# Kernel optimization log

Measured on AMD Instinct MI355X. Metric: run time of the kernel, lower is better.

## Reference

```python
import jax, jax.numpy as jnp
import numpy as np

H, W = 512, 512  # image_size from init_kwargs


def _render_single(xyz, color, opacity):
    """Faithful JAX version of GaussianRenderer._fallback_render (the path the
    module executes when the CUDA rasterizer is unavailable), vectorized.
    Point-splat each Gaussian to one pixel, depth-sort descending (back-to-front),
    alpha-composite: a_k = o_k * prod_{j<k}(1 - o_j); depth = z of front-most hit.
    xyz: (N,3)  color: (N,3)  opacity: (N,1)
    """
    N = xyz.shape[0]
    focal = (H + W) / 2.0
    z = xyz[:, 2]
    xf = xyz[:, 0] / (z + 1e-6) * focal + W / 2.0
    yf = xyz[:, 1] / (z + 1e-6) * focal + H / 2.0
    # torch .long() truncates toward zero
    xi = jnp.trunc(jnp.clip(xf, -1e9, 1e9)).astype(jnp.int32)
    yi = jnp.trunc(jnp.clip(yf, -1e9, 1e9)).astype(jnp.int32)
    valid = (xi >= 0) & (xi < W) & (yi >= 0) & (yi < H)
    pix = jnp.where(valid, yi * W + xi, H * W)  # dummy slot H*W for out-of-bounds
    # stable sort: primary pixel ascending, secondary z descending (back-to-front)
    order = jnp.lexsort((-z, pix))
    pix_s, z_s = pix[order], z[order]
    o_s = opacity[order, 0]
    c_s = color[order]
    valid_s = pix_s < H * W
    # per-pixel exclusive transmittance: alpha recurrence 1-A_k = (1-A_{k-1})(1-o_k)
    logt = jnp.log(jnp.clip(1.0 - o_s, 1e-12, None))
    cs = jnp.cumsum(logt)
    excl = cs - logt  # exclusive cumsum (global)
    start = jnp.concatenate([jnp.ones((1,), bool), pix_s[1:] != pix_s[:-1]])
    start_idx = jax.lax.cummax(jnp.where(start, jnp.arange(N), -1))
    T_prev = jnp.exp(excl - excl[start_idx])  # exclusive within pixel segment
    a = jnp.where(valid_s, o_s * T_prev, 0.0)
    img = jnp.zeros((H * W + 1, 3), xyz.dtype).at[pix_s].add(a[:, None] * c_s)
    # depth: last element written per pixel (front-most, smallest z in segment)
    end = jnp.concatenate([pix_s[1:] != pix_s[:-1], jnp.ones((1,), bool)])
    dpix = jnp.where(end & valid_s, pix_s, H * W)
    depth = jnp.zeros((H * W + 1,), xyz.dtype).at[dpix].set(z_s)
    render = img[: H * W].reshape(H, W, 3).transpose(2, 0, 1)  # (3,H,W)
    return render, depth[: H * W].reshape(1, H, W)


def setup_inputs() -> dict:
    key = jax.random.key(0)
    ks = jax.random.split(key, 5)
    B, N = 8, 262144
    return {
        "xyz": jax.random.normal(ks[0], (B, N, 3), jnp.float32),
        "scale": jax.random.normal(ks[1], (B, N, 3), jnp.float32),
        "rotation": jax.random.normal(ks[2], (B, N, 1), jnp.float32),
        "opacity": jax.random.uniform(ks[3], (B, N, 1), jnp.float32),
        "color": jax.random.uniform(ks[4], (B, N, 3), jnp.float32),
    }


def reference(xyz, scale, rotation, opacity, color):
    # scale/rotation are accepted (part of the gaussians dict) but unused by the
    # fallback renderer, matching the torch source.
    render, depth = jax.vmap(_render_single)(xyz, color, opacity)
    return render, depth
```

## Files before the change

### kernel.cpp

```cpp
#include <hip/hip_runtime.h>
#include <stdint.h>

#define W_ 512
#define H_ 512
#define HW_ (512 * 512)
#define RMAX 4
#define OVF_CAP 65536

__device__ __forceinline__ int project_pix(float x, float y, float z) {
    float zz = z + 1e-6f;
    float xf = x / zz * 512.0f + 256.0f;
    float yf = y / zz * 512.0f + 256.0f;
    xf = fminf(fmaxf(xf, -1e9f), 1e9f);
    yf = fminf(fmaxf(yf, -1e9f), 1e9f);
    int xi = (int)xf;
    int yi = (int)yf;
    if (xi >= 0 && xi < W_ && yi >= 0 && yi < H_) return yi * W_ + xi;
    return -1;
}

__device__ __forceinline__ unsigned int q8(float v) {
    v = fminf(fmaxf(v, 0.f), 1.f);
    return (unsigned int)__float2uint_rn(v * 255.0f);
}
__device__ __forceinline__ float d8(unsigned int u) {
    return (float)(u & 255u) * (1.0f / 255.0f);
}

__global__ void __launch_bounds__(256) k_init(uint4* __restrict__ p, int n4) {
    int i = blockIdx.x * blockDim.x + threadIdx.x;
    if (i < n4) p[i] = make_uint4(0u, 0u, 0u, 0u);
}

__global__ void __launch_bounds__(256) k_build(const float4* __restrict__ xyz4,
                                               const float4* __restrict__ op4,
                                               const float4* __restrict__ col4,
                                               unsigned int* __restrict__ cnt,
                                               unsigned long long* __restrict__ slots,
                                               unsigned int* __restrict__ ovf_hdr,
                                               unsigned int* __restrict__ ovf_pix,
                                               unsigned long long* __restrict__ ovf_rec,
                                               int N, int total4) {
    int t = blockIdx.x * blockDim.x + threadIdx.x;
    if (t >= total4) return;
    float4 v0 = xyz4[3 * (size_t)t + 0];
    float4 v1 = xyz4[3 * (size_t)t + 1];
    float4 v2 = xyz4[3 * (size_t)t + 2];
    float4 o4 = op4[t];
    float4 c0 = col4[3 * (size_t)t + 0];
    float4 c1 = col4[3 * (size_t)t + 1];
    float4 c2 = col4[3 * (size_t)t + 2];
    float xs[4] = {v0.x, v0.w, v1.z, v2.y};
    float ys[4] = {v0.y, v1.x, v1.w, v2.z};
    float zs[4] = {v0.z, v1.y, v2.x, v2.w};
    float os[4] = {o4.x, o4.y, o4.z, o4.w};
    float cr[4] = {c0.x, c0.w, c1.z, c2.y};
    float cg[4] = {c0.y, c1.x, c1.w, c2.z};
    float cb[4] = {c0.z, c1.y, c2.x, c2.w};
    int g0 = 4 * t;
    size_t pbase = (size_t)(g0 / N) * HW_;
#pragma unroll
    for (int j = 0; j < 4; ++j) {
        int pix = project_pix(xs[j], ys[j], zs[j]);
        if (pix >= 0) {
            size_t p = pbase + pix;
            unsigned int sh = 16u * (unsigned int)(p & 1);
            unsigned int old = atomicAdd(&cnt[p >> 1], 1u << sh);
            unsigned int s = (old >> sh) & 0xffffu;
            unsigned int pay = q8(os[j]) | (q8(cr[j]) << 8) | (q8(cg[j]) << 16) |
                               (q8(cb[j]) << 24);
            unsigned long long rec =
                ((unsigned long long)__float_as_uint(zs[j]) << 32) | (unsigned long long)pay;
            if (s < RMAX) {
                slots[p * RMAX + s] = rec;
            } else {
                unsigned int i = atomicAdd(ovf_hdr, 1u);
                if (i < OVF_CAP) { ovf_pix[i] = (unsigned int)p; ovf_rec[i] = rec; }
            }
        }
    }
}

__global__ void __launch_bounds__(256) k_composite(const unsigned int* __restrict__ cnt,
                                                   const unsigned long long* __restrict__ slots,
                                                   const unsigned int* __restrict__ ovf_hdr,
                                                   const unsigned int* __restrict__ ovf_pix,
                                                   const unsigned long long* __restrict__ ovf_rec,
                                                   float* __restrict__ out, int B) {
    int q = blockIdx.x * blockDim.x + threadIdx.x;
    int nb8 = B * (HW_ / 8);
    if (q >= nb8) return;
    int p0 = 8 * q;
    int b = p0 / HW_;
    int pl0 = p0 - b * HW_;

    uint4 cw = ((const uint4*)cnt)[q];
    unsigned int ws[4] = {cw.x, cw.y, cw.z, cw.w};

    float rr[8], gg[8], bb[8], dd[8];

#pragma unroll
    for (int j = 0; j < 8; ++j) {
        unsigned int k = (ws[j >> 1] >> (16 * (j & 1))) & 0xffffu;
        float r = 0.f, g2 = 0.f, bl = 0.f, depth = 0.f;
        if (k > 0) {
            size_t p = (size_t)p0 + j;
            const uint4* sp = (const uint4*)&slots[p * RMAX];
            uint4 s01 = sp[0];
            if (k <= RMAX) {
                uint4 s23 = (k > 2) ? sp[1]
                                    : make_uint4(~0u, 0xff800000u, ~0u, 0xff800000u);
                float z_[4];
                unsigned int y_[4];
                z_[0] = __uint_as_float(s01.y); y_[0] = s01.x;
                z_[1] = (k > 1) ? __uint_as_float(s01.w) : -__builtin_inff();
                y_[1] = s01.z;
                z_[2] = __uint_as_float(s23.y); y_[2] = s23.x;
                z_[3] = (k > 3) ? __uint_as_float(s23.w) : -__builtin_inff();
                y_[3] = s23.z;
#define CE(I, J)                                                                \
                {                                                               \
                    bool sw = (z_[J] > z_[I]) || (z_[J] == z_[I] && y_[J] < y_[I]); \
                    if (sw) {                                                   \
                        float tz = z_[I]; z_[I] = z_[J]; z_[J] = tz;            \
                        unsigned int ty = y_[I]; y_[I] = y_[J]; y_[J] = ty;     \
                    }                                                           \
                }
                CE(0,1) CE(2,3) CE(0,2) CE(1,3) CE(1,2)
#undef CE
                float T = 1.f;
#pragma unroll
                for (int s = 0; s < RMAX; ++s) {
                    if (s < (int)k) {
                        unsigned int pay = y_[s];
                        float o = d8(pay);
                        float a = o * T;
                        r  += a * d8(pay >> 8);
                        g2 += a * d8(pay >> 16);
                        bl += a * d8(pay >> 24);
                        T *= (1.0f - o);
                        depth = z_[s];
                    }
                }
            } else {
                uint4 s23 = sp[1];
                unsigned int nov = ovf_hdr[0];
                if (nov > OVF_CAP) nov = OVF_CAP;
                unsigned int ptag = (unsigned int)p;
                float zz0 = __uint_as_float(s01.y), zz1 = __uint_as_float(s01.w);
                float zz2 = __uint_as_float(s23.y), zz3 = __uint_as_float(s23.w);
                float prev_z = __builtin_inff();
                unsigned int prev_y = 0u;
                float T = 1.f;
                for (int s = 0; s < (int)k; ++s) {
                    float best_z = -__builtin_inff();
                    unsigned int best_y = ~0u;
#define CAND(Z, Y)                                                                   \
                    {                                                                \
                        float z = (Z); unsigned int y = (Y);                         \
                        bool after  = (z < prev_z) || (z == prev_z && y > prev_y);   \
                        bool better = (z > best_z) || (z == best_z && y < best_y);   \
                        if (after && better) { best_z = z; best_y = y; }             \
                    }
                    CAND(zz0, s01.x) CAND(zz1, s01.z) CAND(zz2, s23.x) CAND(zz3, s23.z)
                    for (unsigned int t2 = 0; t2 < nov; ++t2) {
                        if (ovf_pix[t2] == ptag) {
                            unsigned long long rec = ovf_rec[t2];
                            CAND(__uint_as_float((unsigned int)(rec >> 32)),
                                 (unsigned int)rec)
                        }
                    }
#undef CAND
                    unsigned int pay = best_y;
                    float o = d8(pay);
                    float a = o * T;
                    r  += a * d8(pay >> 8);
                    g2 += a * d8(pay >> 16);
                    bl += a * d8(pay >> 24);
                    T *= (1.0f - o);
                    depth = best_z;
                    prev_z = best_z;
                    prev_y = best_y;
                }
            }
        }
        rr[j] = r; gg[j] = g2; bb[j] = bl; dd[j] = depth;
    }

    size_t HWs = (size_t)HW_;
    float* oR = out + ((size_t)b * 3 + 0) * HWs + pl0;
    float* oG = out + ((size_t)b * 3 + 1) * HWs + pl0;
    float* oB = out + ((size_t)b * 3 + 2) * HWs + pl0;
    float* oD = out + (size_t)B * 3 * HWs + (size_t)b * HWs + pl0;
    *(float4*)(oR)     = make_float4(rr[0], rr[1], rr[2], rr[3]);
    *(float4*)(oR + 4) = make_float4(rr[4], rr[5], rr[6], rr[7]);
    *(float4*)(oG)     = make_float4(gg[0], gg[1], gg[2], gg[3]);
    *(float4*)(oG + 4) = make_float4(gg[4], gg[5], gg[6], gg[7]);
    *(float4*)(oB)     = make_float4(bb[0], bb[1], bb[2], bb[3]);
    *(float4*)(oB + 4) = make_float4(bb[4], bb[5], bb[6], bb[7]);
    *(float4*)(oD)     = make_float4(dd[0], dd[1], dd[2], dd[3]);
    *(float4*)(oD + 4) = make_float4(dd[4], dd[5], dd[6], dd[7]);
}

extern "C" void kernel_launch(void* const* d_in, const int* in_sizes, int n_in,
                              void* d_out, int out_size, void* d_ws, size_t ws_size,
                              hipStream_t stream) {
    const float* xyz     = (const float*)d_in[0];
    const float* opacity = (const float*)d_in[3];
    const float* color   = (const float*)d_in[4];
    float* out = (float*)d_out;

    int B = out_size / (4 * HW_);
    int N = in_sizes[0] / (3 * B);
    int total = B * N;
    int nb = B * HW_;

    unsigned int* cnt      = (unsigned int*)d_ws;
    unsigned int* ovf_hdr  = cnt + nb / 2;
    unsigned int* ovf_pix  = ovf_hdr + 64;
    unsigned long long* ovf_rec = (unsigned long long*)(ovf_pix + OVF_CAP);
    unsigned long long* slots   = ovf_rec + OVF_CAP;

    int blk = 256;
    int zwords = nb / 2 + 64;
    int z4 = zwords / 4;
    k_init<<<(z4 + blk - 1) / blk, blk, 0, stream>>>((uint4*)cnt, z4);

    int total4 = total / 4;
    k_build<<<(total4 + blk - 1) / blk, blk, 0, stream>>>((const float4*)xyz,
                                                          (const float4*)opacity,
                                                          (const float4*)color,
                                                          cnt, slots, ovf_hdr, ovf_pix, ovf_rec,
                                                          N, total4);

    int nb8 = nb / 8;
    k_composite<<<(nb8 + blk - 1) / blk, blk, 0, stream>>>(cnt, slots, ovf_hdr, ovf_pix,
                                                           ovf_rec, out, B);
}
```

Measured before the change: 43.06 us.

## Split compositing into zero-fill scan plus compacted work-queue pass

After: 90.15 us. 109% more time.

```diff
diff --git a/kernel.cpp b/kernel.cpp
--- a/kernel.cpp
+++ b/kernel.cpp
@@ -37,7 +37,7 @@
                                                const float4* __restrict__ col4,
                                                unsigned int* __restrict__ cnt,
                                                unsigned long long* __restrict__ slots,
-                                               unsigned int* __restrict__ ovf_hdr,
+                                               unsigned int* __restrict__ hdr,
                                                unsigned int* __restrict__ ovf_pix,
                                                unsigned long long* __restrict__ ovf_rec,
                                                int N, int total4) {
@@ -74,18 +74,16 @@
             if (s < RMAX) {
                 slots[p * RMAX + s] = rec;
             } else {
-                unsigned int i = atomicAdd(ovf_hdr, 1u);
+                unsigned int i = atomicAdd(&hdr[0], 1u);
                 if (i < OVF_CAP) { ovf_pix[i] = (unsigned int)p; ovf_rec[i] = rec; }
             }
         }
     }
 }
 
-__global__ void __launch_bounds__(256) k_composite(const unsigned int* __restrict__ cnt,
-                                                   const unsigned long long* __restrict__ slots,
-                                                   const unsigned int* __restrict__ ovf_hdr,
-                                                   const unsigned int* __restrict__ ovf_pix,
-                                                   const unsigned long long* __restrict__ ovf_rec,
+__global__ void __launch_bounds__(256) k_zero_scan(const unsigned int* __restrict__ cnt,
+                                                   unsigned int* __restrict__ qn,
+                                                   unsigned int* __restrict__ queue,
                                                    float* __restrict__ out, int B) {
     int q = blockIdx.x * blockDim.x + threadIdx.x;
     int nb8 = B * (HW_ / 8);
@@ -97,109 +95,147 @@
     uint4 cw = ((const uint4*)cnt)[q];
     unsigned int ws[4] = {cw.x, cw.y, cw.z, cw.w};
 
-    float rr[8], gg[8], bb[8], dd[8];
-
-#pragma unroll
-    for (int j = 0; j < 8; ++j) {
-        unsigned int k = (ws[j >> 1] >> (16 * (j & 1))) & 0xffffu;
-        float r = 0.f, g2 = 0.f, bl = 0.f, depth = 0.f;
-        if (k > 0) {
-            size_t p = (size_t)p0 + j;
-            const uint4* sp = (const uint4*)&slots[p * RMAX];
-            uint4 s01 = sp[0];
-            if (k <= RMAX) {
-                uint4 s23 = (k > 2) ? sp[1]
-                                    : make_uint4(~0u, 0xff800000u, ~0u, 0xff800000u);
-                float z_[4];
-                unsigned int y_[4];
-                z_[0] = __uint_as_float(s01.y); y_[0] = s01.x;
-                z_[1] = (k > 1) ? __uint_as_float(s01.w) : -__builtin_inff();
-                y_[1] = s01.z;
-                z_[2] = __uint_as_float(s23.y); y_[2] = s23.x;
-                z_[3] = (k > 3) ? __uint_as_float(s23.w) : -__builtin_inff();
-                y_[3] = s23.z;
-#define CE(I, J)                                                                \
-                {                                                               \
-                    bool sw = (z_[J] > z_[I]) || (z_[J] == z_[I] && y_[J] < y_[I]); \
-                    if (sw) {                                                   \
-                        float tz = z_[I]; z_[I] = z_[J]; z_[J] = tz;            \
-                        unsigned int ty = y_[I]; y_[I] = y_[J]; y_[J] = ty;     \
-                    }                                                           \
-                }
-                CE(0,1) CE(2,3) CE(0,2) CE(1,3) CE(1,2)
-#undef CE
-                float T = 1.f;
-#pragma unroll
-                for (int s = 0; s < RMAX; ++s) {
-                    if (s < (int)k) {
-                        unsigned int pay = y_[s];
-                        float o = d8(pay);
-                        float a = o * T;
-                        r  += a * d8(pay >> 8);
-                        g2 += a * d8(pay >> 16);
-                        bl += a * d8(pay >> 24);
-                        T *= (1.0f - o);
-                        depth = z_[s];
-                    }
-                }
-            } else {
-                uint4 s23 = sp[1];
-                unsigned int nov = ovf_hdr[0];
-                if (nov > OVF_CAP) nov = OVF_CAP;
-                unsigned int ptag = (unsigned int)p;
-                float zz0 = __uint_as_float(s01.y), zz1 = __uint_as_float(s01.w);
-                float zz2 = __uint_as_float(s23.y), zz3 = __uint_as_float(s23.w);
-                float prev_z = __builtin_inff();
-                unsigned int prev_y = 0u;
-                float T = 1.f;
-                for (int s = 0; s < (int)k; ++s) {
-                    float best_z = -__builtin_inff();
-                    unsigned int best_y = ~0u;
-#define CAND(Z, Y)                                                                   \
-                    {                                                                \
-                        float z = (Z); unsigned int y = (Y);                         \
-                        bool after  = (z < prev_z) || (z == prev_z && y > prev_y);   \
-                        bool better = (z > best_z) || (z == best_z && y < best_y);   \
-                        if (after && better) { best_z = z; best_y = y; }             \
-                    }
-                    CAND(zz0, s01.x) CAND(zz1, s01.z) CAND(zz2, s23.x) CAND(zz3, s23.z)
-                    for (unsigned int t2 = 0; t2 < nov; ++t2) {
-                        if (ovf_pix[t2] == ptag) {
-                            unsigned long long rec = ovf_rec[t2];
-                            CAND(__uint_as_float((unsigned int)(rec >> 32)),
-                                 (unsigned int)rec)
-                        }
-                    }
-#undef CAND
-                    unsigned int pay = best_y;
-                    float o = d8(pay);
-                    float a = o * T;
-                    r  += a * d8(pay >> 8);
-                    g2 += a * d8(pay >> 16);
-                    bl += a * d8(pay >> 24);
-                    T *= (1.0f - o);
-                    depth = best_z;
-                    prev_z = best_z;
-                    prev_y = best_y;
-                }
-            }
-        }
-        rr[j] = r; gg[j] = g2; bb[j] = bl; dd[j] = depth;
-    }
-
     size_t HWs = (size_t)HW_;
     float* oR = out + ((size_t)b * 3 + 0) * HWs + pl0;
     float* oG = out + ((size_t)b * 3 + 1) * HWs + pl0;
     float* oB = out + ((size_t)b * 3 + 2) * HWs + pl0;
     float* oD = out + (size_t)B * 3 * HWs + (size_t)b * HWs + pl0;
-    *(float4*)(oR)     = make_float4(rr[0], rr[1], rr[2], rr[3]);
-    *(float4*)(oR + 4) = make_float4(rr[4], rr[5], rr[6], rr[7]);
-    *(float4*)(oG)     = make_float4(gg[0], gg[1], gg[2], gg[3]);
-    *(float4*)(oG + 4) = make_float4(gg[4], gg[5], gg[6], gg[7]);
-    *(float4*)(oB)     = make_float4(bb[0], bb[1], bb[2], bb[3]);
-    *(float4*)(oB + 4) = make_float4(bb[4], bb[5], bb[6], bb[7]);
-    *(float4*)(oD)     = make_float4(dd[0], dd[1], dd[2], dd[3]);
-    *(float4*)(oD + 4) = make_float4(dd[4], dd[5], dd[6], dd[7]);
+    float4 z4 = make_float4(0.f, 0.f, 0.f, 0.f);
+    *(float4*)(oR) = z4; *(float4*)(oR + 4) = z4;
+    *(float4*)(oG) = z4; *(float4*)(oG + 4) = z4;
+    *(float4*)(oB) = z4; *(float4*)(oB + 4) = z4;
+    *(float4*)(oD) = z4; *(float4*)(oD + 4) = z4;
+
+    unsigned int m = 0;
+#pragma unroll
+    for (int j = 0; j < 8; ++j)
+        m += ((ws[j >> 1] >> (16 * (j & 1))) & 0xffffu) ? 1u : 0u;
+
+    int lane = threadIdx.x & 63;
+    unsigned int incl = m;
+#pragma unroll
+    for (int d = 1; d < 64; d <<= 1) {
+        unsigned int v = __shfl_up(incl, d, 64);
+        if (lane >= d) incl += v;
+    }
+    unsigned int total = __shfl(incl, 63, 64);
+    if (total == 0) return;
+    unsigned int wbase = 0;
+    if (lane == 63) wbase = atomicAdd(qn, incl);
+    wbase = __shfl(wbase, 63, 64);
+    unsigned int mybase = wbase + incl - m;
+
+#pragma unroll
+    for (int j = 0; j < 8; ++j) {
+        unsigned int k = (ws[j >> 1] >> (16 * (j & 1))) & 0xffffu;
+        if (k) {
+            unsigned int kc = k < 2047u ? k : 2047u;
+            queue[mybase++] = (kc << 21) | (unsigned int)(p0 + j);
+        }
+    }
+}
+
+__global__ void __launch_bounds__(256) k_body(const unsigned int* __restrict__ cnt,
+                                              const unsigned long long* __restrict__ slots,
+                                              const unsigned int* __restrict__ hdr,
+                                              const unsigned int* __restrict__ ovf_pix,
+                                              const unsigned long long* __restrict__ ovf_rec,
+                                              const unsigned int* __restrict__ qn,
+                                              const unsigned int* __restrict__ queue,
+                                              float* __restrict__ out, int B) {
+    unsigned int i = blockIdx.x * blockDim.x + threadIdx.x;
+    if (i >= qn[0]) return;
+    unsigned int e = queue[i];
+    unsigned int k = e >> 21;
+    unsigned int p = e & 0x1fffffu;
+
+    const uint4* sp = (const uint4*)&slots[(size_t)p * RMAX];
+    uint4 s01 = sp[0];
+    float r = 0.f, g2 = 0.f, bl = 0.f, depth = 0.f;
+
+    if (k <= RMAX) {
+        uint4 s23 = (k > 2) ? sp[1] : make_uint4(~0u, 0xff800000u, ~0u, 0xff800000u);
+        float z_[4];
+        unsigned int y_[4];
+        z_[0] = __uint_as_float(s01.y); y_[0] = s01.x;
+        z_[1] = (k > 1) ? __uint_as_float(s01.w) : -__builtin_inff();
+        y_[1] = s01.z;
+        z_[2] = __uint_as_float(s23.y); y_[2] = s23.x;
+        z_[3] = (k > 3) ? __uint_as_float(s23.w) : -__builtin_inff();
+        y_[3] = s23.z;
+#define CE(I, J)                                                            \
+        {                                                                   \
+            bool sw = (z_[J] > z_[I]) || (z_[J] == z_[I] && y_[J] < y_[I]); \
+            if (sw) {                                                       \
+                float tz = z_[I]; z_[I] = z_[J]; z_[J] = tz;                \
+                unsigned int ty = y_[I]; y_[I] = y_[J]; y_[J] = ty;         \
+            }                                                               \
+        }
+        CE(0,1) CE(2,3) CE(0,2) CE(1,3) CE(1,2)
+#undef CE
+        float T = 1.f;
+#pragma unroll
+        for (int s = 0; s < RMAX; ++s) {
+            if (s < (int)k) {
+                unsigned int pay = y_[s];
+                float o = d8(pay);
+                float a = o * T;
+                r  += a * d8(pay >> 8);
+                g2 += a * d8(pay >> 16);
+                bl += a * d8(pay >> 24);
+                T *= (1.0f - o);
+                depth = z_[s];
+            }
+        }
+    } else {
+        unsigned int shp = 16u * (p & 1u);
+        int kk = (int)((cnt[p >> 1] >> shp) & 0xffffu);
+        uint4 s23 = sp[1];
+        unsigned int nov = hdr[0];
+        if (nov > OVF_CAP) nov = OVF_CAP;
+        float zz0 = __uint_as_float(s01.y), zz1 = __uint_as_float(s01.w);
+        float zz2 = __uint_as_float(s23.y), zz3 = __uint_as_float(s23.w);
+        float prev_z = __builtin_inff();
+        unsigned int prev_y = 0u;
+        float T = 1.f;
+        for (int s = 0; s < kk; ++s) {
+            float best_z = -__builtin_inff();
+            unsigned int best_y = ~0u;
+#define CAND(Z, Y)                                                               \
+            {                                                                    \
+                float z = (Z); unsigned int y = (Y);                             \
+                bool after  = (z < prev_z) || (z == prev_z && y > prev_y);       \
+                bool better = (z > best_z) || (z == best_z && y < best_y);       \
+                if (after && better) { best_z = z; best_y = y; }                 \
+            }
+            CAND(zz0, s01.x) CAND(zz1, s01.z) CAND(zz2, s23.x) CAND(zz3, s23.z)
+            for (unsigned int t2 = 0; t2 < nov; ++t2) {
+                if (ovf_pix[t2] == p) {
+                    unsigned long long rec = ovf_rec[t2];
+                    CAND(__uint_as_float((unsigned int)(rec >> 32)), (unsigned int)rec)
+                }
+            }
+#undef CAND
+            unsigned int pay = best_y;
+            float o = d8(pay);
+            float a = o * T;
+            r  += a * d8(pay >> 8);
+            g2 += a * d8(pay >> 16);
+            bl += a * d8(pay >> 24);
+            T *= (1.0f - o);
+            depth = best_z;
+            prev_z = best_z;
+            prev_y = best_y;
+        }
+    }
+
+    int b = p / HW_;
+    int pl = p - b * HW_;
+    size_t HWs = (size_t)HW_;
+    out[((size_t)b * 3 + 0) * HWs + pl] = r;
+    out[((size_t)b * 3 + 1) * HWs + pl] = g2;
+    out[((size_t)b * 3 + 2) * HWs + pl] = bl;
+    out[(size_t)B * 3 * HWs + (size_t)b * HWs + pl] = depth;
 }
 
 extern "C" void kernel_launch(void* const* d_in, const int* in_sizes, int n_in,
@@ -215,11 +251,12 @@
     int total = B * N;
     int nb = B * HW_;
 
-    unsigned int* cnt      = (unsigned int*)d_ws;
-    unsigned int* ovf_hdr  = cnt + nb / 2;
-    unsigned int* ovf_pix  = ovf_hdr + 64;
+    unsigned int* cnt     = (unsigned int*)d_ws;
+    unsigned int* hdr     = cnt + nb / 2;
+    unsigned int* ovf_pix = hdr + 64;
     unsigned long long* ovf_rec = (unsigned long long*)(ovf_pix + OVF_CAP);
     unsigned long long* slots   = ovf_rec + OVF_CAP;
+    unsigned int* queue   = (unsigned int*)(slots + (size_t)nb * RMAX);
 
     int blk = 256;
     int zwords = nb / 2 + 64;
@@ -230,10 +267,12 @@
     k_build<<<(total4 + blk - 1) / blk, blk, 0, stream>>>((const float4*)xyz,
                                                           (const float4*)opacity,
                                                           (const float4*)color,
-                                                          cnt, slots, ovf_hdr, ovf_pix, ovf_rec,
+                                                          cnt, slots, hdr, ovf_pix, ovf_rec,
                                                           N, total4);
 
     int nb8 = nb / 8;
-    k_composite<<<(nb8 + blk - 1) / blk, blk, 0, stream>>>(cnt, slots, ovf_hdr, ovf_pix,
-                                                           ovf_rec, out, B);
-}
+    k_zero_scan<<<(nb8 + blk - 1) / blk, blk, 0, stream>>>(cnt, &hdr[1], queue, out, B);
+
+    k_body<<<(nb + blk - 1) / blk, blk, 0, stream>>>(cnt, slots, hdr, ovf_pix, ovf_rec,
+                                                     &hdr[1], queue, out, B);
+}
```
